# Optimization experiments

Measured on AMD Instinct MI355X. Metric: run time of the kernel, lower is better.

The kernel has to match this reference:

```python
import jax, jax.numpy as jnp
import numpy as np

B, N, D, D_MODEL = 4, 2048, 512, 512


def setup_inputs() -> dict:
    key = jax.random.key(0)
    kx, kq, kk, kv, ks = jax.random.split(key, 5)
    scale = 1.0 / np.sqrt(D)
    x = jax.random.normal(kx, (B, N, D), dtype=jnp.float32)
    Wq = (jax.random.normal(kq, (D, D_MODEL), dtype=jnp.float32) * scale)
    Wk = (jax.random.normal(kk, (D, D_MODEL), dtype=jnp.float32) * scale)
    Wv = (jax.random.normal(kv, (D, D_MODEL), dtype=jnp.float32) * scale)
    Ws = (jax.random.normal(ks, (D, 1), dtype=jnp.float32) * scale)
    return {"x": x, "Wq": Wq, "Wk": Wk, "Wv": Wv, "Ws": Ws}


def reference(x, Wq, Wk, Wv, Ws):
    # Projections (Linear, no bias)
    Q = x @ Wq                      # (B, N, d_model)
    K = x @ Wk                      # (B, N, d_model)
    V = x @ Wv                      # (B, N, d_model)
    sigma = x @ Ws                  # (B, N, 1)

    n = x.shape[1]
    dm = Wq.shape[1]

    # Prior association: Gaussian kernel over |i-j| distance, row-normalized
    idx = jnp.arange(n)
    dist = jnp.abs(idx[:, None] - idx[None, :]).astype(x.dtype)      # (N, N)
    inv_norm = 1.0 / (jnp.sqrt(2.0 * jnp.pi).astype(x.dtype) * jnp.abs(sigma))
    gaussian = inv_norm * jnp.exp(-0.5 * jnp.square(dist[None] / sigma))  # (B,N,N)
    P = gaussian / jnp.sum(gaussian, axis=-1, keepdims=True)

    # Series association: scaled dot-product softmax attention
    scores = jnp.einsum('bnd,bmd->bnm', Q, K) / jnp.sqrt(jnp.asarray(dm, x.dtype))
    S = jax.nn.softmax(scores, axis=-1)                               # (B,N,N)

    # Reconstruction
    Z = S @ V                                                          # (B,N,d_model)
    return (Z, P)
```

## Files before the change

kernel.cpp:

```cpp
#include <hip/hip_runtime.h>

typedef float f32x4 __attribute__((ext_vector_type(4)));
typedef short s16x8 __attribute__((ext_vector_type(8)));
typedef unsigned short us4 __attribute__((ext_vector_type(4)));

#define MFMA16(a, b, c) __builtin_amdgcn_mfma_f32_16x16x32_bf16(a, b, c, 0, 0, 0)

#define GLOAD_LDS16(gp, lp) __builtin_amdgcn_global_load_lds( \
    (__attribute__((address_space(1))) void*)(gp),            \
    (__attribute__((address_space(3))) void*)(lp), 16, 0, 0)

__device__ __forceinline__ unsigned short f2bf(float f) {
    union { float f; unsigned u; } v; v.f = f;
    unsigned r = v.u + 0x7fffu + ((v.u >> 16) & 1u);
    return (unsigned short)(r >> 16);
}

#define RP 136
#define SH128 (128 * RP)

__device__ __forceinline__ void gemm_core128_cnt(
    const unsigned short* __restrict__ Ab, size_t Astride,
    const unsigned short* __restrict__ Bb, size_t Bstride,
    int K, unsigned short* sh, int t, f32x4 acc[4][4])
{
    const int wave = t >> 6, lane = t & 63;
    const int c = lane & 15, quad = lane >> 4;
    const int wm = (wave >> 1) * 64, wn = (wave & 1) * 64;
    const int srow = t >> 2;
    const int scol = (t & 3) * 8;

    const unsigned short* ga = Ab + (size_t)srow * Astride + scol;
    const unsigned short* gb = Bb + (size_t)srow * Bstride + scol;

    GLOAD_LDS16(ga,                 sh + t * 8);
    GLOAD_LDS16(ga + 64 * Astride,  sh + 2048 + t * 8);
    GLOAD_LDS16(gb,                 sh + 4096 + t * 8);
    GLOAD_LDS16(gb + 64 * Bstride,  sh + 6144 + t * 8);
    if (32 < K) {
        GLOAD_LDS16(ga + 32,                 sh + 8192 + t * 8);
        GLOAD_LDS16(ga + 32 + 64 * Astride,  sh + 8192 + 2048 + t * 8);
        GLOAD_LDS16(gb + 32,                 sh + 8192 + 4096 + t * 8);
        GLOAD_LDS16(gb + 32 + 64 * Bstride,  sh + 8192 + 6144 + t * 8);
    }

    int cur = 0;
    for (int k0 = 0; k0 < K; k0 += 32) {
        if (k0 + 32 < K) asm volatile("s_waitcnt vmcnt(4)" ::: "memory");
        else             asm volatile("s_waitcnt vmcnt(0)" ::: "memory");
        __builtin_amdgcn_s_barrier();
        __builtin_amdgcn_sched_barrier(0);

        const unsigned short* buf = sh + cur * 8192;
        s16x8 af[4], bf[4];
        #pragma unroll
        for (int i = 0; i < 4; i++)
            af[i] = *(const s16x8*)(buf + (wm + i * 16 + c) * 32 + quad * 8);
        #pragma unroll
        for (int i = 0; i < 4; i++)
            bf[i] = *(const s16x8*)(buf + 4096 + (wn + i * 16 + c) * 32 + quad * 8);

        asm volatile("s_waitcnt lgkmcnt(0)" ::: "memory");
        __builtin_amdgcn_sched_barrier(0);

        #pragma unroll
        for (int mt = 0; mt < 4; mt++)
            #pragma unroll
            for (int nt = 0; nt < 4; nt++)
                acc[mt][nt] = MFMA16(af[mt], bf[nt], acc[mt][nt]);

        __builtin_amdgcn_s_barrier();
        __builtin_amdgcn_sched_barrier(0);

        if (k0 + 64 < K) {
            unsigned short* nb = sh + cur * 8192;
            GLOAD_LDS16(ga + k0 + 64,                 nb + t * 8);
            GLOAD_LDS16(ga + k0 + 64 + 64 * Astride,  nb + 2048 + t * 8);
            GLOAD_LDS16(gb + k0 + 64,                 nb + 4096 + t * 8);
            GLOAD_LDS16(gb + k0 + 64 + 64 * Bstride,  nb + 6144 + t * 8);
        }
        cur ^= 1;
    }
}

__global__ __launch_bounds__(256) void k_convert(
    const float* __restrict__ x, const float* __restrict__ wq,
    const float* __restrict__ wk, const float* __restrict__ wv,
    unsigned short* __restrict__ xbf, unsigned short* __restrict__ wt)
{
    __shared__ __align__(16) unsigned short lt[64][72];

    int bid = blockIdx.x, t = threadIdx.x;
    if (bid < 4096) {
        int gid = bid * 256 + t;
        float4 v = ((const float4*)x)[gid];
        us4 o = { f2bf(v.x), f2bf(v.y), f2bf(v.z), f2bf(v.w) };
        ((us4*)xbf)[gid] = o;
    } else {
        int idx = bid - 4096;
        int w = idx >> 6;
        int tile = idx & 63;
        int tk = tile >> 3, tn = tile & 7;
        const float* src = ((w == 0) ? wq : (w == 1) ? wk : wv)
                         + (size_t)(tk * 64) * 512 + tn * 64;

        int row = t >> 2;
        int c0 = (t & 3) * 16;
        const float4* s = (const float4*)(src + (size_t)row * 512 + c0);
        #pragma unroll
        for (int q = 0; q < 4; q++) {
            float4 v = s[q];
            lt[c0 + q * 4 + 0][row] = f2bf(v.x);
            lt[c0 + q * 4 + 1][row] = f2bf(v.y);
            lt[c0 + q * 4 + 2][row] = f2bf(v.z);
            lt[c0 + q * 4 + 3][row] = f2bf(v.w);
        }
        __syncthreads();

        int n = t >> 2;
        int k0 = (t & 3) * 16;
        s16x8 a = *(const s16x8*)&lt[n][k0];
        s16x8 b = *(const s16x8*)&lt[n][k0 + 8];
        unsigned short* dst = wt + (((size_t)(w * 512 + tn * 64 + n)) << 9)
                                 + tk * 64 + k0;
        *(s16x8*)dst = a;
        *(s16x8*)(dst + 8) = b;
    }
}

__global__ __launch_bounds__(256) void k_proj(
    const unsigned short* __restrict__ xbf, const unsigned short* __restrict__ wt,
    unsigned short* __restrict__ qbf, unsigned short* __restrict__ kbf,
    unsigned short* __restrict__ vtbf)
{
    __shared__ __align__(16) unsigned short sh[SH128];

    int t = threadIdx.x;
    int m0 = blockIdx.x * 128, n0 = blockIdx.y * 128;
    f32x4 acc[4][4] = {};

    gemm_core128_cnt(xbf + (size_t)m0 * 512, 512, wt + (size_t)n0 * 512, 512,
                     512, sh, t, acc);

    int wave = t >> 6, lane = t & 63, c = lane & 15, quad = lane >> 4;
    int wm = (wave >> 1) * 64, wn = (wave & 1) * 64;
    int sel = blockIdx.y >> 2;

    if (sel < 2) {
        unsigned short* dst = sel ? kbf : qbf;
        int ncol0 = n0 - sel * 512;
        #pragma unroll
        for (int mt = 0; mt < 4; mt++)
            #pragma unroll
            for (int nt = 0; nt < 4; nt++)
                #pragma unroll
                for (int r = 0; r < 4; r++)
                    sh[(wm + mt * 16 + quad * 4 + r) * RP + wn + nt * 16 + c]
                        = f2bf(acc[mt][nt][r]);
        __syncthreads();
        int rr = t >> 1, hh = (t & 1) * 64;
        const s16x8* sp = (const s16x8*)(sh + rr * RP + hh);
        s16x8* dp = (s16x8*)(dst + (size_t)(m0 + rr) * 512 + ncol0 + hh);
        s16x8 v[8];
        #pragma unroll
        for (int i = 0; i < 8; i++) v[i] = sp[i];
        #pragma unroll
        for (int i = 0; i < 8; i++) dp[i] = v[i];
    } else {
        #pragma unroll
        for (int mt = 0; mt < 4; mt++)
            #pragma unroll
            for (int nt = 0; nt < 4; nt++)
                #pragma unroll
                for (int r = 0; r < 4; r++)
                    sh[(wn + nt * 16 + c) * RP + wm + mt * 16 + quad * 4 + r]
                        = f2bf(acc[mt][nt][r]);
        __syncthreads();
        int bb = m0 >> 11, nn0 = m0 & 2047;
        int dbase = n0 - 1024;
        int dl = t >> 1, nh = (t & 1) * 64;
        const s16x8* sp = (const s16x8*)(sh + dl * RP + nh);
        s16x8* dp = (s16x8*)(vtbf + ((size_t)(bb * 512 + dbase + dl)) * 2048
                                  + nn0 + nh);
        s16x8 v[8];
        #pragma unroll
        for (int i = 0; i < 8; i++) v[i] = sp[i];
        #pragma unroll
        for (int i = 0; i < 8; i++) dp[i] = v[i];
    }
}

__device__ __forceinline__ void score_body(
    const unsigned short* __restrict__ qbf, const unsigned short* __restrict__ kbf,
    unsigned short* __restrict__ pbf,
    int b, int m0, int n0, int t, unsigned short* sh)
{
    f32x4 acc[4][4] = {};
    gemm_core128_cnt(qbf + (size_t)(b * 2048 + m0) * 512, 512,
                     kbf + (size_t)(b * 2048 + n0) * 512, 512,
                     512, sh, t, acc);

    int wave = t >> 6, lane = t & 63, c = lane & 15, quad = lane >> 4;
    int wm = (wave >> 1) * 64, wn = (wave & 1) * 64;
    const float scale = 0.044194173824159216f;

    #pragma unroll
    for (int mt = 0; mt < 4; mt++) {
        #pragma unroll
        for (int r = 0; r < 4; r++) {
            int row = wm + mt * 16 + quad * 4 + r;
            #pragma unroll
            for (int nt = 0; nt < 4; nt++) {
                float p = __expf(acc[mt][nt][r] * scale);
                sh[row * RP + wn + nt * 16 + c] = f2bf(p);
            }
        }
    }
    __syncthreads();
    int rr = t >> 1, hh = (t & 1) * 64;
    const s16x8* sp = (const s16x8*)(sh + rr * RP + hh);
    s16x8* dp = (s16x8*)(pbf + (size_t)(b * 2048 + m0 + rr) * 2048 + n0 + hh);
    s16x8 v[8];
    #pragma unroll
    for (int i = 0; i < 8; i++) v[i] = sp[i];
    #pragma unroll
    for (int i = 0; i < 8; i++) dp[i] = v[i];
}

__device__ __forceinline__ void prior_wave(
    const float* __restrict__ x, const float* __restrict__ wsv,
    float* __restrict__ pout, int row, int lane)
{
    const float4* xr = (const float4*)(x + (size_t)row * 512);
    const float4* wr = (const float4*)wsv;
    float4 a0 = xr[lane * 2],     b0 = wr[lane * 2];
    float4 a1 = xr[lane * 2 + 1], b1 = wr[lane * 2 + 1];
    float part = a0.x * b0.x + a0.y * b0.y + a0.z * b0.z + a0.w * b0.w
               + a1.x * b1.x + a1.y * b1.y + a1.z * b1.z + a1.w * b1.w;
    #pragma unroll
    for (int o = 32; o; o >>= 1) part += __shfl_xor(part, o, 64);
    float sigma = part;
    float inv2 = 0.5f / (sigma * sigma);

    int i = row & 2047;
    float g[32];
    float sum = 0.f;
    #pragma unroll
    for (int u = 0; u < 8; u++) {
        #pragma unroll
        for (int v = 0; v < 4; v++) {
            float d = (float)(u * 256 + lane * 4 + v - i);
            float e = __expf(-(d * d) * inv2);
            g[u * 4 + v] = e;
            sum += e;
        }
    }
    #pragma unroll
    for (int o = 32; o; o >>= 1) sum += __shfl_xor(sum, o, 64);
    float inv = 1.0f / sum;

    float4* pr = (float4*)(pout + (size_t)row * 2048);
    #pragma unroll
    for (int u = 0; u < 8; u++) {
        float4 o4 = { g[u * 4] * inv, g[u * 4 + 1] * inv,
                      g[u * 4 + 2] * inv, g[u * 4 + 3] * inv };
        pr[u * 64 + lane] = o4;
    }
}

__global__ __launch_bounds__(256) void k_score_prior(
    const unsigned short* __restrict__ qbf, const unsigned short* __restrict__ kbf,
    unsigned short* __restrict__ pbf,
    const float* __restrict__ x, const float* __restrict__ wsv,
    float* __restrict__ pout)
{
    __shared__ __align__(16) unsigned short sh[SH128];

    int bid = blockIdx.x, t = threadIdx.x;
    if (bid < 1024) {
        int b = bid >> 8, r = bid & 255;
        score_body(qbf, kbf, pbf, b, (r & 15) * 128, (r >> 4) * 128, t, sh);
    } else {
        int row = (bid - 1024) * 4 + (t >> 6);
        prior_wave(x, wsv, pout, row, t & 63);
    }
}

__global__ __launch_bounds__(256) void k_score(
    const unsigned short* __restrict__ qbf, const unsigned short* __restrict__ kbf,
    unsigned short* __restrict__ pbf)
{
    __shared__ __align__(16) unsigned short sh[SH128];
    score_body(qbf, kbf, pbf, blockIdx.z,
               blockIdx.x * 128, blockIdx.y * 128, threadIdx.x, sh);
}

__global__ __launch_bounds__(256) void k_out(
    const unsigned short* __restrict__ pbf, const unsigned short* __restrict__ vtbf,
    float* __restrict__ zout)
{
    __shared__ __align__(16) unsigned short sh[12288];

    int t = threadIdx.x;
    int b = blockIdx.z;
    int m0 = blockIdx.x * 128, n0 = blockIdx.y * 64;

    const int wave = t >> 6, lane = t & 63;
    const int c = lane & 15, quad = lane >> 4;
    const int wm = (wave >> 1) * 64, wn = (wave & 1) * 32;
    const int srow = t >> 2;
    const int scol = (t & 3) * 8;

    const unsigned short* ga = pbf + (size_t)(b * 2048 + m0 + srow) * 2048 + scol;
    const unsigned short* gb = vtbf + (size_t)(b * 512 + n0 + srow) * 2048 + scol;

    s16x8 ones;
    #pragma unroll
    for (int i = 0; i < 8; i++) ones[i] = (short)0x3F80;

    f32x4 acc[4][2] = {};
    f32x4 accl[4] = {};

    GLOAD_LDS16(ga,                  sh + t * 8);
    GLOAD_LDS16(ga + 64 * 2048,      sh + 2048 + t * 8);
    GLOAD_LDS16(gb,                  sh + 4096 + t * 8);
    GLOAD_LDS16(ga + 32,             sh + 6144 + t * 8);
    GLOAD_LDS16(ga + 32 + 64 * 2048, sh + 6144 + 2048 + t * 8);
    GLOAD_LDS16(gb + 32,             sh + 6144 + 4096 + t * 8);

    int cur = 0;
    for (int k0 = 0; k0 < 2048; k0 += 32) {
        if (k0 + 32 < 2048) asm volatile("s_waitcnt vmcnt(3)" ::: "memory");
        else                asm volatile("s_waitcnt vmcnt(0)" ::: "memory");
        __builtin_amdgcn_s_barrier();
        __builtin_amdgcn_sched_barrier(0);

        const unsigned short* buf = sh + cur * 6144;
        s16x8 af[4], bf[2];
        #pragma unroll
        for (int i = 0; i < 4; i++)
            af[i] = *(const s16x8*)(buf + (wm + i * 16 + c) * 32 + quad * 8);
        #pragma unroll
        for (int i = 0; i < 2; i++)
            bf[i] = *(const s16x8*)(buf + 4096 + (wn + i * 16 + c) * 32 + quad * 8);

        asm volatile("s_waitcnt lgkmcnt(0)" ::: "memory");
        __builtin_amdgcn_sched_barrier(0);

        #pragma unroll
        for (int mt = 0; mt < 4; mt++) {
            #pragma unroll
            for (int nt = 0; nt < 2; nt++)
                acc[mt][nt] = MFMA16(af[mt], bf[nt], acc[mt][nt]);
            accl[mt] = MFMA16(af[mt], ones, accl[mt]);
        }

        __builtin_amdgcn_s_barrier();
        __builtin_amdgcn_sched_barrier(0);

        if (k0 + 64 < 2048) {
            unsigned short* nb = sh + cur * 6144;
            GLOAD_LDS16(ga + k0 + 64,             nb + t * 8);
            GLOAD_LDS16(ga + k0 + 64 + 64 * 2048, nb + 2048 + t * 8);
            GLOAD_LDS16(gb + k0 + 64,             nb + 4096 + t * 8);
        }
        cur ^= 1;
    }

    #pragma unroll
    for (int mt = 0; mt < 4; mt++) {
        #pragma unroll
        for (int r = 0; r < 4; r++) {
            int row = wm + mt * 16 + quad * 4 + r;
            float inv = 1.0f / accl[mt][r];
            #pragma unroll
            for (int nt = 0; nt < 2; nt++) {
                zout[(size_t)(b * 2048 + m0 + row) * 512 + n0 + wn + nt * 16 + c]
                    = acc[mt][nt][r] * inv;
            }
        }
    }
}

__global__ __launch_bounds__(256) void k_prior(
    const float* __restrict__ x, const float* __restrict__ wsv,
    float* __restrict__ pout)
{
    int row = blockIdx.x * 4 + (threadIdx.x >> 6);
    prior_wave(x, wsv, pout, row, threadIdx.x & 63);
}

extern "C" void kernel_launch(void* const* d_in, const int* in_sizes, int n_in,
                              void* d_out, int out_size, void* d_ws, size_t ws_size,
                              hipStream_t stream)
{
    const float* x  = (const float*)d_in[0];
    const float* wq = (const float*)d_in[1];
    const float* wk = (const float*)d_in[2];
    const float* wv = (const float*)d_in[3];
    const float* ws = (const float*)d_in[4];

    float* zout = (float*)d_out;
    float* pout = zout + (size_t)4 * 2048 * 512;

    const size_t need = ((size_t)4194304 + 786432 + 3 * 4194304 + 16777216) * 2;

    if (ws_size >= need) {
        unsigned short* base = (unsigned short*)d_ws;
        unsigned short* xbf  = base;
        unsigned short* wt   = xbf  + (size_t)4194304;
        unsigned short* qbf  = wt   + (size_t)786432;
        unsigned short* kbf  = qbf  + (size_t)4194304;
        unsigned short* vtbf = kbf  + (size_t)4194304;
        unsigned short* pbf  = vtbf + (size_t)4194304;

        k_convert<<<dim3(4288), dim3(256), 0, stream>>>(x, wq, wk, wv, xbf, wt);
        k_proj       <<<dim3(64, 12),   dim3(256), 0, stream>>>(xbf, wt, qbf, kbf, vtbf);
        k_score_prior<<<dim3(3072),     dim3(256), 0, stream>>>(qbf, kbf, pbf, x, ws, pout);
        k_out        <<<dim3(16, 8, 4), dim3(256), 0, stream>>>(pbf, vtbf, zout);
    } else {
        unsigned short* base = (unsigned short*)pout;
        unsigned short* pbf  = base;
        unsigned short* qbf  = base + (size_t)16777216;
        unsigned short* kbf  = qbf  + (size_t)4194304;
        unsigned short* vtbf = kbf  + (size_t)4194304;
        unsigned short* xbf  = base;
        unsigned short* wt   = base + (size_t)4194304;

        k_convert<<<dim3(4288), dim3(256), 0, stream>>>(x, wq, wk, wv, xbf, wt);
        k_proj  <<<dim3(64, 12),    dim3(256), 0, stream>>>(xbf, wt, qbf, kbf, vtbf);
        k_score <<<dim3(16, 16, 4), dim3(256), 0, stream>>>(qbf, kbf, pbf);
        k_out   <<<dim3(16, 8, 4),  dim3(256), 0, stream>>>(pbf, vtbf, zout);
        k_prior <<<dim3(2048),      dim3(256), 0, stream>>>(x, ws, pout);
    }
}
```

Before: 198.2 us.

## Triple-buffer GEMM K-loops, swizzle block order, move prior into convert kernel

Every MFMA GEMM loop (projection, score, output) now keeps three LDS stages in flight instead of two, with vmcnt waits adjusted to match. This is meant to hide more global-load latency. Grids are flattened to 1D with an XCD-aware swizzle (blockIdx & 7) so that neighbouring tiles share L2 on the same die. The Gaussian prior computation moves out of the score kernel and into the convert kernel, so the score kernel runs GEMM only. The cost is more LDS per block (48 KB for the 128x128 GEMMs), which may reduce occupancy.

```diff
diff --git a/kernel.cpp b/kernel.cpp
--- a/kernel.cpp
+++ b/kernel.cpp
@@ -17,9 +17,9 @@
 }
 
 #define RP 136
-#define SH128 (128 * RP)
-
-__device__ __forceinline__ void gemm_core128_cnt(
+#define SH128 24576
+
+__device__ __forceinline__ void gemm_core128_p3(
     const unsigned short* __restrict__ Ab, size_t Astride,
     const unsigned short* __restrict__ Bb, size_t Bstride,
     int K, unsigned short* sh, int t, f32x4 acc[4][4])
@@ -32,33 +32,33 @@
 
     const unsigned short* ga = Ab + (size_t)srow * Astride + scol;
     const unsigned short* gb = Bb + (size_t)srow * Bstride + scol;
-
-    GLOAD_LDS16(ga,                 sh + t * 8);
-    GLOAD_LDS16(ga + 64 * Astride,  sh + 2048 + t * 8);
-    GLOAD_LDS16(gb,                 sh + 4096 + t * 8);
-    GLOAD_LDS16(gb + 64 * Bstride,  sh + 6144 + t * 8);
-    if (32 < K) {
-        GLOAD_LDS16(ga + 32,                 sh + 8192 + t * 8);
-        GLOAD_LDS16(ga + 32 + 64 * Astride,  sh + 8192 + 2048 + t * 8);
-        GLOAD_LDS16(gb + 32,                 sh + 8192 + 4096 + t * 8);
-        GLOAD_LDS16(gb + 32 + 64 * Bstride,  sh + 8192 + 6144 + t * 8);
+    const int nt = K >> 5;
+
+    for (int p = 0; p < 3 && p < nt; p++) {
+        unsigned short* nb = sh + p * 8192;
+        GLOAD_LDS16(ga + p * 32,                 nb + t * 8);
+        GLOAD_LDS16(ga + p * 32 + 64 * Astride,  nb + 2048 + t * 8);
+        GLOAD_LDS16(gb + p * 32,                 nb + 4096 + t * 8);
+        GLOAD_LDS16(gb + p * 32 + 64 * Bstride,  nb + 6144 + t * 8);
     }
 
     int cur = 0;
-    for (int k0 = 0; k0 < K; k0 += 32) {
-        if (k0 + 32 < K) asm volatile("s_waitcnt vmcnt(4)" ::: "memory");
-        else             asm volatile("s_waitcnt vmcnt(0)" ::: "memory");
+    for (int i = 0; i < nt; i++) {
+        int rem = nt - 1 - i;
+        if (rem >= 2)      asm volatile("s_waitcnt vmcnt(8)" ::: "memory");
+        else if (rem == 1) asm volatile("s_waitcnt vmcnt(4)" ::: "memory");
+        else               asm volatile("s_waitcnt vmcnt(0)" ::: "memory");
         __builtin_amdgcn_s_barrier();
         __builtin_amdgcn_sched_barrier(0);
 
         const unsigned short* buf = sh + cur * 8192;
         s16x8 af[4], bf[4];
         #pragma unroll
-        for (int i = 0; i < 4; i++)
-            af[i] = *(const s16x8*)(buf + (wm + i * 16 + c) * 32 + quad * 8);
-        #pragma unroll
-        for (int i = 0; i < 4; i++)
-            bf[i] = *(const s16x8*)(buf + 4096 + (wn + i * 16 + c) * 32 + quad * 8);
+        for (int q = 0; q < 4; q++)
+            af[q] = *(const s16x8*)(buf + (wm + q * 16 + c) * 32 + quad * 8);
+        #pragma unroll
+        for (int q = 0; q < 4; q++)
+            bf[q] = *(const s16x8*)(buf + 4096 + (wn + q * 16 + c) * 32 + quad * 8);
 
         asm volatile("s_waitcnt lgkmcnt(0)" ::: "memory");
         __builtin_amdgcn_sched_barrier(0);
@@ -66,31 +66,71 @@
         #pragma unroll
         for (int mt = 0; mt < 4; mt++)
             #pragma unroll
-            for (int nt = 0; nt < 4; nt++)
-                acc[mt][nt] = MFMA16(af[mt], bf[nt], acc[mt][nt]);
+            for (int ntl = 0; ntl < 4; ntl++)
+                acc[mt][ntl] = MFMA16(af[mt], bf[ntl], acc[mt][ntl]);
 
         __builtin_amdgcn_s_barrier();
         __builtin_amdgcn_sched_barrier(0);
 
-        if (k0 + 64 < K) {
+        if (i + 3 < nt) {
             unsigned short* nb = sh + cur * 8192;
-            GLOAD_LDS16(ga + k0 + 64,                 nb + t * 8);
-            GLOAD_LDS16(ga + k0 + 64 + 64 * Astride,  nb + 2048 + t * 8);
-            GLOAD_LDS16(gb + k0 + 64,                 nb + 4096 + t * 8);
-            GLOAD_LDS16(gb + k0 + 64 + 64 * Bstride,  nb + 6144 + t * 8);
-        }
-        cur ^= 1;
-    }
-}
-
-__global__ __launch_bounds__(256) void k_convert(
+            int kk = (i + 3) * 32;
+            GLOAD_LDS16(ga + kk,                 nb + t * 8);
+            GLOAD_LDS16(ga + kk + 64 * Astride,  nb + 2048 + t * 8);
+            GLOAD_LDS16(gb + kk,                 nb + 4096 + t * 8);
+            GLOAD_LDS16(gb + kk + 64 * Bstride,  nb + 6144 + t * 8);
+        }
+        cur = (cur == 2) ? 0 : cur + 1;
+    }
+}
+
+__device__ __forceinline__ void prior_wave(
+    const float* __restrict__ x, const float* __restrict__ wsv,
+    float* __restrict__ pout, int row, int lane)
+{
+    const float4* xr = (const float4*)(x + (size_t)row * 512);
+    const float4* wr = (const float4*)wsv;
+    float4 a0 = xr[lane * 2],     b0 = wr[lane * 2];
+    float4 a1 = xr[lane * 2 + 1], b1 = wr[lane * 2 + 1];
+    float part = a0.x * b0.x + a0.y * b0.y + a0.z * b0.z + a0.w * b0.w
+               + a1.x * b1.x + a1.y * b1.y + a1.z * b1.z + a1.w * b1.w;
+    #pragma unroll
+    for (int o = 32; o; o >>= 1) part += __shfl_xor(part, o, 64);
+    float sigma = part;
+    float inv2 = 0.5f / (sigma * sigma);
+
+    int i = row & 2047;
+    float g[32];
+    float sum = 0.f;
+    #pragma unroll
+    for (int u = 0; u < 8; u++) {
+        #pragma unroll
+        for (int v = 0; v < 4; v++) {
+            float d = (float)(u * 256 + lane * 4 + v - i);
+            float e = __expf(-(d * d) * inv2);
+            g[u * 4 + v] = e;
+            sum += e;
+        }
+    }
+    #pragma unroll
+    for (int o = 32; o; o >>= 1) sum += __shfl_xor(sum, o, 64);
+    float inv = 1.0f / sum;
+
+    float4* pr = (float4*)(pout + (size_t)row * 2048);
+    #pragma unroll
+    for (int u = 0; u < 8; u++) {
+        float4 o4 = { g[u * 4] * inv, g[u * 4 + 1] * inv,
+                      g[u * 4 + 2] * inv, g[u * 4 + 3] * inv };
+        pr[u * 64 + lane] = o4;
+    }
+}
+
+__device__ __forceinline__ void convert_body(
     const float* __restrict__ x, const float* __restrict__ wq,
     const float* __restrict__ wk, const float* __restrict__ wv,
-    unsigned short* __restrict__ xbf, unsigned short* __restrict__ wt)
-{
-    __shared__ __align__(16) unsigned short lt[64][72];
-
-    int bid = blockIdx.x, t = threadIdx.x;
+    unsigned short* __restrict__ xbf, unsigned short* __restrict__ wt,
+    int bid, int t, unsigned short (*lt)[72])
+{
     if (bid < 4096) {
         int gid = bid * 256 + t;
         float4 v = ((const float4*)x)[gid];
@@ -128,6 +168,31 @@
     }
 }
 
+__global__ __launch_bounds__(256) void k_convert_prior(
+    const float* __restrict__ x, const float* __restrict__ wq,
+    const float* __restrict__ wk, const float* __restrict__ wv,
+    unsigned short* __restrict__ xbf, unsigned short* __restrict__ wt,
+    const float* __restrict__ wsv, float* __restrict__ pout)
+{
+    __shared__ __align__(16) unsigned short lt[64][72];
+    int bid = blockIdx.x, t = threadIdx.x;
+    if (bid < 4288) {
+        convert_body(x, wq, wk, wv, xbf, wt, bid, t, lt);
+    } else {
+        int row = (bid - 4288) * 4 + (t >> 6);
+        prior_wave(x, wsv, pout, row, t & 63);
+    }
+}
+
+__global__ __launch_bounds__(256) void k_convert(
+    const float* __restrict__ x, const float* __restrict__ wq,
+    const float* __restrict__ wk, const float* __restrict__ wv,
+    unsigned short* __restrict__ xbf, unsigned short* __restrict__ wt)
+{
+    __shared__ __align__(16) unsigned short lt[64][72];
+    convert_body(x, wq, wk, wv, xbf, wt, blockIdx.x, threadIdx.x, lt);
+}
+
 __global__ __launch_bounds__(256) void k_proj(
     const unsigned short* __restrict__ xbf, const unsigned short* __restrict__ wt,
     unsigned short* __restrict__ qbf, unsigned short* __restrict__ kbf,
@@ -136,15 +201,18 @@
     __shared__ __align__(16) unsigned short sh[SH128];
 
     int t = threadIdx.x;
-    int m0 = blockIdx.x * 128, n0 = blockIdx.y * 128;
+    int lin = blockIdx.x;
+    int sw = (lin & 7) * 96 + (lin >> 3);
+    int mt_ = sw / 12, nt_ = sw % 12;
+    int m0 = mt_ * 128, n0 = nt_ * 128;
     f32x4 acc[4][4] = {};
 
-    gemm_core128_cnt(xbf + (size_t)m0 * 512, 512, wt + (size_t)n0 * 512, 512,
-                     512, sh, t, acc);
+    gemm_core128_p3(xbf + (size_t)m0 * 512, 512, wt + (size_t)n0 * 512, 512,
+                    512, sh, t, acc);
 
     int wave = t >> 6, lane = t & 63, c = lane & 15, quad = lane >> 4;
     int wm = (wave >> 1) * 64, wn = (wave & 1) * 64;
-    int sel = blockIdx.y >> 2;
+    int sel = nt_ >> 2;
 
     if (sel < 2) {
         unsigned short* dst = sel ? kbf : qbf;
@@ -190,15 +258,21 @@
     }
 }
 
-__device__ __forceinline__ void score_body(
+__global__ __launch_bounds__(256) void k_score(
     const unsigned short* __restrict__ qbf, const unsigned short* __restrict__ kbf,
-    unsigned short* __restrict__ pbf,
-    int b, int m0, int n0, int t, unsigned short* sh)
-{
+    unsigned short* __restrict__ pbf)
+{
+    __shared__ __align__(16) unsigned short sh[SH128];
+
+    int t = threadIdx.x;
+    int sw = (blockIdx.x & 7) * 128 + (blockIdx.x >> 3);
+    int b = sw >> 8, r = sw & 255;
+    int m0 = (r >> 4) * 128, n0 = (r & 15) * 128;
+
     f32x4 acc[4][4] = {};
-    gemm_core128_cnt(qbf + (size_t)(b * 2048 + m0) * 512, 512,
-                     kbf + (size_t)(b * 2048 + n0) * 512, 512,
-                     512, sh, t, acc);
+    gemm_core128_p3(qbf + (size_t)(b * 2048 + m0) * 512, 512,
+                    kbf + (size_t)(b * 2048 + n0) * 512, 512,
+                    512, sh, t, acc);
 
     int wave = t >> 6, lane = t & 63, c = lane & 15, quad = lane >> 4;
     int wm = (wave >> 1) * 64, wn = (wave & 1) * 64;
@@ -207,11 +281,11 @@
     #pragma unroll
     for (int mt = 0; mt < 4; mt++) {
         #pragma unroll
-        for (int r = 0; r < 4; r++) {
-            int row = wm + mt * 16 + quad * 4 + r;
+        for (int r2 = 0; r2 < 4; r2++) {
+            int row = wm + mt * 16 + quad * 4 + r2;
             #pragma unroll
             for (int nt = 0; nt < 4; nt++) {
-                float p = __expf(acc[mt][nt][r] * scale);
+                float p = __expf(acc[mt][nt][r2] * scale);
                 sh[row * RP + wn + nt * 16 + c] = f2bf(p);
             }
         }
@@ -227,83 +301,16 @@
     for (int i = 0; i < 8; i++) dp[i] = v[i];
 }
 
-__device__ __forceinline__ void prior_wave(
-    const float* __restrict__ x, const float* __restrict__ wsv,
-    float* __restrict__ pout, int row, int lane)
-{
-    const float4* xr = (const float4*)(x + (size_t)row * 512);
-    const float4* wr = (const float4*)wsv;
-    float4 a0 = xr[lane * 2],     b0 = wr[lane * 2];
-    float4 a1 = xr[lane * 2 + 1], b1 = wr[lane * 2 + 1];
-    float part = a0.x * b0.x + a0.y * b0.y + a0.z * b0.z + a0.w * b0.w
-               + a1.x * b1.x + a1.y * b1.y + a1.z * b1.z + a1.w * b1.w;
-    #pragma unroll
-    for (int o = 32; o; o >>= 1) part += __shfl_xor(part, o, 64);
-    float sigma = part;
-    float inv2 = 0.5f / (sigma * sigma);
-
-    int i = row & 2047;
-    float g[32];
-    float sum = 0.f;
-    #pragma unroll
-    for (int u = 0; u < 8; u++) {
-        #pragma unroll
-        for (int v = 0; v < 4; v++) {
-            float d = (float)(u * 256 + lane * 4 + v - i);
-            float e = __expf(-(d * d) * inv2);
-            g[u * 4 + v] = e;
-            sum += e;
-        }
-    }
-    #pragma unroll
-    for (int o = 32; o; o >>= 1) sum += __shfl_xor(sum, o, 64);
-    float inv = 1.0f / sum;
-
-    float4* pr = (float4*)(pout + (size_t)row * 2048);
-    #pragma unroll
-    for (int u = 0; u < 8; u++) {
-        float4 o4 = { g[u * 4] * inv, g[u * 4 + 1] * inv,
-                      g[u * 4 + 2] * inv, g[u * 4 + 3] * inv };
-        pr[u * 64 + lane] = o4;
-    }
-}
-
-__global__ __launch_bounds__(256) void k_score_prior(
-    const unsigned short* __restrict__ qbf, const unsigned short* __restrict__ kbf,
-    unsigned short* __restrict__ pbf,
-    const float* __restrict__ x, const float* __restrict__ wsv,
-    float* __restrict__ pout)
-{
-    __shared__ __align__(16) unsigned short sh[SH128];
-
-    int bid = blockIdx.x, t = threadIdx.x;
-    if (bid < 1024) {
-        int b = bid >> 8, r = bid & 255;
-        score_body(qbf, kbf, pbf, b, (r & 15) * 128, (r >> 4) * 128, t, sh);
-    } else {
-        int row = (bid - 1024) * 4 + (t >> 6);
-        prior_wave(x, wsv, pout, row, t & 63);
-    }
-}
-
-__global__ __launch_bounds__(256) void k_score(
-    const unsigned short* __restrict__ qbf, const unsigned short* __restrict__ kbf,
-    unsigned short* __restrict__ pbf)
-{
-    __shared__ __align__(16) unsigned short sh[SH128];
-    score_body(qbf, kbf, pbf, blockIdx.z,
-               blockIdx.x * 128, blockIdx.y * 128, threadIdx.x, sh);
-}
-
 __global__ __launch_bounds__(256) void k_out(
     const unsigned short* __restrict__ pbf, const unsigned short* __restrict__ vtbf,
     float* __restrict__ zout)
 {
-    __shared__ __align__(16) unsigned short sh[12288];
+    __shared__ __align__(16) unsigned short sh[18432];
 
     int t = threadIdx.x;
-    int b = blockIdx.z;
-    int m0 = blockIdx.x * 128, n0 = blockIdx.y * 64;
+    int sw = (blockIdx.x & 7) * 64 + (blockIdx.x >> 3);
+    int b = sw >> 7, r = sw & 127;
+    int m0 = (r >> 3) * 128, n0 = (r & 7) * 64;
 
     const int wave = t >> 6, lane = t & 63;
     const int c = lane & 15, quad = lane >> 4;
@@ -321,28 +328,31 @@
     f32x4 acc[4][2] = {};
     f32x4 accl[4] = {};
 
-    GLOAD_LDS16(ga,                  sh + t * 8);
-    GLOAD_LDS16(ga + 64 * 2048,      sh + 2048 + t * 8);
-    GLOAD_LDS16(gb,                  sh + 4096 + t * 8);
-    GLOAD_LDS16(ga + 32,             sh + 6144 + t * 8);
-    GLOAD_LDS16(ga + 32 + 64 * 2048, sh + 6144 + 2048 + t * 8);
-    GLOAD_LDS16(gb + 32,             sh + 6144 + 4096 + t * 8);
+    #pragma unroll
+    for (int p = 0; p < 3; p++) {
+        unsigned short* nb = sh + p * 6144;
+        GLOAD_LDS16(ga + p * 32,             nb + t * 8);
+        GLOAD_LDS16(ga + p * 32 + 64 * 2048, nb + 2048 + t * 8);
+        GLOAD_LDS16(gb + p * 32,             nb + 4096 + t * 8);
+    }
 
     int cur = 0;
-    for (int k0 = 0; k0 < 2048; k0 += 32) {
-        if (k0 + 32 < 2048) asm volatile("s_waitcnt vmcnt(3)" ::: "memory");
-        else                asm volatile("s_waitcnt vmcnt(0)" ::: "memory");
+    for (int i = 0; i < 64; i++) {
+        int rem = 63 - i;
+        if (rem >= 2)      asm volatile("s_waitcnt vmcnt(6)" ::: "memory");
+        else if (rem == 1) asm volatile("s_waitcnt vmcnt(3)" ::: "memory");
+        else               asm volatile("s_waitcnt vmcnt(0)" ::: "memory");
         __builtin_amdgcn_s_barrier();
         __builtin_amdgcn_sched_barrier(0);
 
         const unsigned short* buf = sh + cur * 6144;
         s16x8 af[4], bf[2];
         #pragma unroll
-        for (int i = 0; i < 4; i++)
-            af[i] = *(const s16x8*)(buf + (wm + i * 16 + c) * 32 + quad * 8);
-        #pragma unroll
-        for (int i = 0; i < 2; i++)
-            bf[i] = *(const s16x8*)(buf + 4096 + (wn + i * 16 + c) * 32 + quad * 8);
+        for (int q = 0; q < 4; q++)
+            af[q] = *(const s16x8*)(buf + (wm + q * 16 + c) * 32 + quad * 8);
+        #pragma unroll
+        for (int q = 0; q < 2; q++)
+            bf[q] = *(const s16x8*)(buf + 4096 + (wn + q * 16 + c) * 32 + quad * 8);
 
         asm volatile("s_waitcnt lgkmcnt(0)" ::: "memory");
         __builtin_amdgcn_sched_barrier(0);
@@ -358,25 +368,26 @@
         __builtin_amdgcn_s_barrier();
         __builtin_amdgcn_sched_barrier(0);
 
-        if (k0 + 64 < 2048) {
+        if (i + 3 < 64) {
             unsigned short* nb = sh + cur * 6144;
-            GLOAD_LDS16(ga + k0 + 64,             nb + t * 8);
-            GLOAD_LDS16(ga + k0 + 64 + 64 * 2048, nb + 2048 + t * 8);
-            GLOAD_LDS16(gb + k0 + 64,             nb + 4096 + t * 8);
-        }
-        cur ^= 1;
+            int kk = (i + 3) * 32;
+            GLOAD_LDS16(ga + kk,             nb + t * 8);
+            GLOAD_LDS16(ga + kk + 64 * 2048, nb + 2048 + t * 8);
+            GLOAD_LDS16(gb + kk,             nb + 4096 + t * 8);
+        }
+        cur = (cur == 2) ? 0 : cur + 1;
     }
 
     #pragma unroll
     for (int mt = 0; mt < 4; mt++) {
         #pragma unroll
-        for (int r = 0; r < 4; r++) {
-            int row = wm + mt * 16 + quad * 4 + r;
-            float inv = 1.0f / accl[mt][r];
+        for (int r2 = 0; r2 < 4; r2++) {
+            int row = wm + mt * 16 + quad * 4 + r2;
+            float inv = 1.0f / accl[mt][r2];
             #pragma unroll
             for (int nt = 0; nt < 2; nt++) {
                 zout[(size_t)(b * 2048 + m0 + row) * 512 + n0 + wn + nt * 16 + c]
-                    = acc[mt][nt][r] * inv;
+                    = acc[mt][nt][r2] * inv;
             }
         }
     }
@@ -414,10 +425,11 @@
         unsigned short* vtbf = kbf  + (size_t)4194304;
         unsigned short* pbf  = vtbf + (size_t)4194304;
 
-        k_convert<<<dim3(4288), dim3(256), 0, stream>>>(x, wq, wk, wv, xbf, wt);
-        k_proj       <<<dim3(64, 12),   dim3(256), 0, stream>>>(xbf, wt, qbf, kbf, vtbf);
-        k_score_prior<<<dim3(3072),     dim3(256), 0, stream>>>(qbf, kbf, pbf, x, ws, pout);
-        k_out        <<<dim3(16, 8, 4), dim3(256), 0, stream>>>(pbf, vtbf, zout);
+        k_convert_prior<<<dim3(6336), dim3(256), 0, stream>>>(
+            x, wq, wk, wv, xbf, wt, ws, pout);
+        k_proj <<<dim3(768),  dim3(256), 0, stream>>>(xbf, wt, qbf, kbf, vtbf);
+        k_score<<<dim3(1024), dim3(256), 0, stream>>>(qbf, kbf, pbf);
+        k_out  <<<dim3(512),  dim3(256), 0, stream>>>(pbf, vtbf, zout);
     } else {
         unsigned short* base = (unsigned short*)pout;
         unsigned short* pbf  = base;
@@ -428,9 +440,9 @@
         unsigned short* wt   = base + (size_t)4194304;
 
         k_convert<<<dim3(4288), dim3(256), 0, stream>>>(x, wq, wk, wv, xbf, wt);
-        k_proj  <<<dim3(64, 12),    dim3(256), 0, stream>>>(xbf, wt, qbf, kbf, vtbf);
-        k_score <<<dim3(16, 16, 4), dim3(256), 0, stream>>>(qbf, kbf, pbf);
-        k_out   <<<dim3(16, 8, 4),  dim3(256), 0, stream>>>(pbf, vtbf, zout);
-        k_prior <<<dim3(2048),      dim3(256), 0, stream>>>(x, ws, pout);
-    }
-}
+        k_proj <<<dim3(768),  dim3(256), 0, stream>>>(xbf, wt, qbf, kbf, vtbf);
+        k_score<<<dim3(1024), dim3(256), 0, stream>>>(qbf, kbf, pbf);
+        k_out  <<<dim3(512),  dim3(256), 0, stream>>>(pbf, vtbf, zout);
+        k_prior<<<dim3(2048), dim3(256), 0, stream>>>(x, ws, pout);
+    }
+}
```

Result: slower. 203.1 us (+2.5%).

## Enlarge projection and score GEMM tiles to 256x256 with 512-thread blocks

Applied to the files above, without the earlier changes.

Replaces the 128x128 GEMM core with a 256x256 tile computed by 8 waves, each holding 128x64 of accumulators. This raises arithmetic intensity and cuts global/LDS traffic per FLOP for the projection and score kernels. It also drops the LDS-staged epilogue in favour of direct scalar bf16 stores to global memory. The prior rows are re-batched to 8 per block. The larger tile means more accumulator registers, fewer blocks (256 score blocks on a 256-CU part), and uncoalesced 2-byte epilogue stores, so occupancy and store efficiency may suffer.

```diff
diff --git a/kernel.cpp b/kernel.cpp
--- a/kernel.cpp
+++ b/kernel.cpp
@@ -16,55 +16,55 @@
     return (unsigned short)(r >> 16);
 }
 
-#define RP 136
-#define SH128 (128 * RP)
-
-__device__ __forceinline__ void gemm_core128_cnt(
+__device__ __forceinline__ void gemm_core256(
     const unsigned short* __restrict__ Ab, size_t Astride,
     const unsigned short* __restrict__ Bb, size_t Bstride,
-    int K, unsigned short* sh, int t, f32x4 acc[4][4])
-{
-    const int wave = t >> 6, lane = t & 63;
+    int K, unsigned short* sh, int t, f32x4 acc[8][4])
+{
+    const int w = t >> 6, lane = t & 63;
     const int c = lane & 15, quad = lane >> 4;
-    const int wm = (wave >> 1) * 64, wn = (wave & 1) * 64;
+    const int arow = (w >> 2) * 128;
+    const int brow = (w & 3) * 64;
     const int srow = t >> 2;
     const int scol = (t & 3) * 8;
 
     const unsigned short* ga = Ab + (size_t)srow * Astride + scol;
     const unsigned short* gb = Bb + (size_t)srow * Bstride + scol;
-
-    GLOAD_LDS16(ga,                 sh + t * 8);
-    GLOAD_LDS16(ga + 64 * Astride,  sh + 2048 + t * 8);
-    GLOAD_LDS16(gb,                 sh + 4096 + t * 8);
-    GLOAD_LDS16(gb + 64 * Bstride,  sh + 6144 + t * 8);
-    if (32 < K) {
-        GLOAD_LDS16(ga + 32,                 sh + 8192 + t * 8);
-        GLOAD_LDS16(ga + 32 + 64 * Astride,  sh + 8192 + 2048 + t * 8);
-        GLOAD_LDS16(gb + 32,                 sh + 8192 + 4096 + t * 8);
-        GLOAD_LDS16(gb + 32 + 64 * Bstride,  sh + 8192 + 6144 + t * 8);
-    }
+    const int ntil = K >> 5;
+
+#define STAGE256(p, bbuf) do {                                      \
+        unsigned short* nb = sh + (bbuf) * 16384;                   \
+        int kk = (p) * 32;                                          \
+        GLOAD_LDS16(ga + kk,                 nb + t * 8);           \
+        GLOAD_LDS16(ga + kk + 128 * Astride, nb + 4096 + t * 8);    \
+        GLOAD_LDS16(gb + kk,                 nb + 8192 + t * 8);    \
+        GLOAD_LDS16(gb + kk + 128 * Bstride, nb + 12288 + t * 8);   \
+    } while (0)
+
+    STAGE256(0, 0);
+    STAGE256(1, 1);
 
     int cur = 0;
-    for (int k0 = 0; k0 < K; k0 += 32) {
-        if (k0 + 32 < K) asm volatile("s_waitcnt vmcnt(4)" ::: "memory");
-        else             asm volatile("s_waitcnt vmcnt(0)" ::: "memory");
+    for (int i = 0; i < ntil; i++) {
+        if (i + 1 < ntil) asm volatile("s_waitcnt vmcnt(4)" ::: "memory");
+        else              asm volatile("s_waitcnt vmcnt(0)" ::: "memory");
         __builtin_amdgcn_s_barrier();
         __builtin_amdgcn_sched_barrier(0);
 
-        const unsigned short* buf = sh + cur * 8192;
-        s16x8 af[4], bf[4];
-        #pragma unroll
-        for (int i = 0; i < 4; i++)
-            af[i] = *(const s16x8*)(buf + (wm + i * 16 + c) * 32 + quad * 8);
-        #pragma unroll
-        for (int i = 0; i < 4; i++)
-            bf[i] = *(const s16x8*)(buf + 4096 + (wn + i * 16 + c) * 32 + quad * 8);
+        const unsigned short* buf = sh + cur * 16384;
+        s16x8 af[8], bf[4];
+        #pragma unroll
+        for (int q = 0; q < 8; q++)
+            af[q] = *(const s16x8*)(buf + (arow + q * 16 + c) * 32 + quad * 8);
+        #pragma unroll
+        for (int q = 0; q < 4; q++)
+            bf[q] = *(const s16x8*)(buf + 8192 + (brow + q * 16 + c) * 32 + quad * 8);
 
         asm volatile("s_waitcnt lgkmcnt(0)" ::: "memory");
         __builtin_amdgcn_sched_barrier(0);
 
         #pragma unroll
-        for (int mt = 0; mt < 4; mt++)
+        for (int mt = 0; mt < 8; mt++)
             #pragma unroll
             for (int nt = 0; nt < 4; nt++)
                 acc[mt][nt] = MFMA16(af[mt], bf[nt], acc[mt][nt]);
@@ -72,14 +72,50 @@
         __builtin_amdgcn_s_barrier();
         __builtin_amdgcn_sched_barrier(0);
 
-        if (k0 + 64 < K) {
-            unsigned short* nb = sh + cur * 8192;
-            GLOAD_LDS16(ga + k0 + 64,                 nb + t * 8);
-            GLOAD_LDS16(ga + k0 + 64 + 64 * Astride,  nb + 2048 + t * 8);
-            GLOAD_LDS16(gb + k0 + 64,                 nb + 4096 + t * 8);
-            GLOAD_LDS16(gb + k0 + 64 + 64 * Bstride,  nb + 6144 + t * 8);
-        }
+        if (i + 2 < ntil) STAGE256(i + 2, cur);
         cur ^= 1;
+    }
+#undef STAGE256
+}
+
+__device__ __forceinline__ void prior_wave(
+    const float* __restrict__ x, const float* __restrict__ wsv,
+    float* __restrict__ pout, int row, int lane)
+{
+    const float4* xr = (const float4*)(x + (size_t)row * 512);
+    const float4* wr = (const float4*)wsv;
+    float4 a0 = xr[lane * 2],     b0 = wr[lane * 2];
+    float4 a1 = xr[lane * 2 + 1], b1 = wr[lane * 2 + 1];
+    float part = a0.x * b0.x + a0.y * b0.y + a0.z * b0.z + a0.w * b0.w
+               + a1.x * b1.x + a1.y * b1.y + a1.z * b1.z + a1.w * b1.w;
+    #pragma unroll
+    for (int o = 32; o; o >>= 1) part += __shfl_xor(part, o, 64);
+    float sigma = part;
+    float inv2 = 0.5f / (sigma * sigma);
+
+    int i = row & 2047;
+    float g[32];
+    float sum = 0.f;
+    #pragma unroll
+    for (int u = 0; u < 8; u++) {
+        #pragma unroll
+        for (int v = 0; v < 4; v++) {
+            float d = (float)(u * 256 + lane * 4 + v - i);
+            float e = __expf(-(d * d) * inv2);
+            g[u * 4 + v] = e;
+            sum += e;
+        }
+    }
+    #pragma unroll
+    for (int o = 32; o; o >>= 1) sum += __shfl_xor(sum, o, 64);
+    float inv = 1.0f / sum;
+
+    float4* pr = (float4*)(pout + (size_t)row * 2048);
+    #pragma unroll
+    for (int u = 0; u < 8; u++) {
+        float4 o4 = { g[u * 4] * inv, g[u * 4 + 1] * inv,
+                      g[u * 4 + 2] * inv, g[u * 4 + 3] * inv };
+        pr[u * 64 + lane] = o4;
     }
 }
 
@@ -128,65 +164,53 @@
     }
 }
 
-__global__ __launch_bounds__(256) void k_proj(
+__global__ __launch_bounds__(512, 2) void k_proj(
     const unsigned short* __restrict__ xbf, const unsigned short* __restrict__ wt,
     unsigned short* __restrict__ qbf, unsigned short* __restrict__ kbf,
     unsigned short* __restrict__ vtbf)
 {
-    __shared__ __align__(16) unsigned short sh[SH128];
+    __shared__ __align__(16) unsigned short sh[32768];
 
     int t = threadIdx.x;
-    int m0 = blockIdx.x * 128, n0 = blockIdx.y * 128;
-    f32x4 acc[4][4] = {};
-
-    gemm_core128_cnt(xbf + (size_t)m0 * 512, 512, wt + (size_t)n0 * 512, 512,
-                     512, sh, t, acc);
-
-    int wave = t >> 6, lane = t & 63, c = lane & 15, quad = lane >> 4;
-    int wm = (wave >> 1) * 64, wn = (wave & 1) * 64;
-    int sel = blockIdx.y >> 2;
+    int mt_ = blockIdx.x / 6, nt_ = blockIdx.x % 6;
+    int m0 = mt_ * 256, n0 = nt_ * 256;
+
+    f32x4 acc[8][4] = {};
+    gemm_core256(xbf + (size_t)m0 * 512, 512, wt + (size_t)n0 * 512, 512,
+                 512, sh, t, acc);
+
+    int w = t >> 6, lane = t & 63, c = lane & 15, quad = lane >> 4;
+    int wr = w >> 2, wc = w & 3;
+    int sel = nt_ >> 1;
 
     if (sel < 2) {
         unsigned short* dst = sel ? kbf : qbf;
         int ncol0 = n0 - sel * 512;
         #pragma unroll
-        for (int mt = 0; mt < 4; mt++)
-            #pragma unroll
-            for (int nt = 0; nt < 4; nt++)
+        for (int mt = 0; mt < 8; mt++) {
+            #pragma unroll
+            for (int nt = 0; nt < 4; nt++) {
+                int col = ncol0 + wc * 64 + nt * 16 + c;
                 #pragma unroll
-                for (int r = 0; r < 4; r++)
-                    sh[(wm + mt * 16 + quad * 4 + r) * RP + wn + nt * 16 + c]
-                        = f2bf(acc[mt][nt][r]);
-        __syncthreads();
-        int rr = t >> 1, hh = (t & 1) * 64;
-        const s16x8* sp = (const s16x8*)(sh + rr * RP + hh);
-        s16x8* dp = (s16x8*)(dst + (size_t)(m0 + rr) * 512 + ncol0 + hh);
-        s16x8 v[8];
-        #pragma unroll
-        for (int i = 0; i < 8; i++) v[i] = sp[i];
-        #pragma unroll
-        for (int i = 0; i < 8; i++) dp[i] = v[i];
+                for (int r = 0; r < 4; r++) {
+                    int rw = m0 + wr * 128 + mt * 16 + quad * 4 + r;
+                    dst[(size_t)rw * 512 + col] = f2bf(acc[mt][nt][r]);
+                }
+            }
+        }
     } else {
         #pragma unroll
-        for (int mt = 0; mt < 4; mt++)
-            #pragma unroll
-            for (int nt = 0; nt < 4; nt++)
-                #pragma unroll
-                for (int r = 0; r < 4; r++)
-                    sh[(wn + nt * 16 + c) * RP + wm + mt * 16 + quad * 4 + r]
-                        = f2bf(acc[mt][nt][r]);
-        __syncthreads();
-        int bb = m0 >> 11, nn0 = m0 & 2047;
-        int dbase = n0 - 1024;
-        int dl = t >> 1, nh = (t & 1) * 64;
-        const s16x8* sp = (const s16x8*)(sh + dl * RP + nh);
-        s16x8* dp = (s16x8*)(vtbf + ((size_t)(bb * 512 + dbase + dl)) * 2048
-                                  + nn0 + nh);
-        s16x8 v[8];
-        #pragma unroll
-        for (int i = 0; i < 8; i++) v[i] = sp[i];
-        #pragma unroll
-        for (int i = 0; i < 8; i++) dp[i] = v[i];
+        for (int mt = 0; mt < 8; mt++) {
+            int rw0 = m0 + wr * 128 + mt * 16 + quad * 4;
+            int bb = rw0 >> 11, nn = rw0 & 2047;
+            #pragma unroll
+            for (int nt = 0; nt < 4; nt++) {
+                int d = (n0 - 1024) + wc * 64 + nt * 16 + c;
+                us4 pk = { f2bf(acc[mt][nt][0]), f2bf(acc[mt][nt][1]),
+                           f2bf(acc[mt][nt][2]), f2bf(acc[mt][nt][3]) };
+                *(us4*)(vtbf + ((size_t)(bb * 512 + d)) * 2048 + nn) = pk;
+            }
+        }
     }
 }
 
@@ -195,104 +219,57 @@
     unsigned short* __restrict__ pbf,
     int b, int m0, int n0, int t, unsigned short* sh)
 {
-    f32x4 acc[4][4] = {};
-    gemm_core128_cnt(qbf + (size_t)(b * 2048 + m0) * 512, 512,
-                     kbf + (size_t)(b * 2048 + n0) * 512, 512,
-                     512, sh, t, acc);
-
-    int wave = t >> 6, lane = t & 63, c = lane & 15, quad = lane >> 4;
-    int wm = (wave >> 1) * 64, wn = (wave & 1) * 64;
+    f32x4 acc[8][4] = {};
+    gemm_core256(qbf + (size_t)(b * 2048 + m0) * 512, 512,
+                 kbf + (size_t)(b * 2048 + n0) * 512, 512,
+                 512, sh, t, acc);
+
+    int w = t >> 6, lane = t & 63, c = lane & 15, quad = lane >> 4;
+    int wr = w >> 2, wc = w & 3;
     const float scale = 0.044194173824159216f;
 
     #pragma unroll
-    for (int mt = 0; mt < 4; mt++) {
-        #pragma unroll
-        for (int r = 0; r < 4; r++) {
-            int row = wm + mt * 16 + quad * 4 + r;
-            #pragma unroll
-            for (int nt = 0; nt < 4; nt++) {
-                float p = __expf(acc[mt][nt][r] * scale);
-                sh[row * RP + wn + nt * 16 + c] = f2bf(p);
+    for (int mt = 0; mt < 8; mt++) {
+        #pragma unroll
+        for (int nt = 0; nt < 4; nt++) {
+            int col = n0 + wc * 64 + nt * 16 + c;
+            #pragma unroll
+            for (int r = 0; r < 4; r++) {
+                int row = m0 + wr * 128 + mt * 16 + quad * 4 + r;
+                pbf[(size_t)(b * 2048 + row) * 2048 + col]
+                    = f2bf(__expf(acc[mt][nt][r] * scale));
             }
         }
     }
-    __syncthreads();
-    int rr = t >> 1, hh = (t & 1) * 64;
-    const s16x8* sp = (const s16x8*)(sh + rr * RP + hh);
-    s16x8* dp = (s16x8*)(pbf + (size_t)(b * 2048 + m0 + rr) * 2048 + n0 + hh);
-    s16x8 v[8];
-    #pragma unroll
-    for (int i = 0; i < 8; i++) v[i] = sp[i];
-    #pragma unroll
-    for (int i = 0; i < 8; i++) dp[i] = v[i];
-}
-
-__device__ __forceinline__ void prior_wave(
-    const float* __restrict__ x, const float* __restrict__ wsv,
-    float* __restrict__ pout, int row, int lane)
-{
-    const float4* xr = (const float4*)(x + (size_t)row * 512);
-    const float4* wr = (const float4*)wsv;
-    float4 a0 = xr[lane * 2],     b0 = wr[lane * 2];
-    float4 a1 = xr[lane * 2 + 1], b1 = wr[lane * 2 + 1];
-    float part = a0.x * b0.x + a0.y * b0.y + a0.z * b0.z + a0.w * b0.w
-               + a1.x * b1.x + a1.y * b1.y + a1.z * b1.z + a1.w * b1.w;
-    #pragma unroll
-    for (int o = 32; o; o >>= 1) part += __shfl_xor(part, o, 64);
-    float sigma = part;
-    float inv2 = 0.5f / (sigma * sigma);
-
-    int i = row & 2047;
-    float g[32];
-    float sum = 0.f;
-    #pragma unroll
-    for (int u = 0; u < 8; u++) {
-        #pragma unroll
-        for (int v = 0; v < 4; v++) {
-            float d = (float)(u * 256 + lane * 4 + v - i);
-            float e = __expf(-(d * d) * inv2);
-            g[u * 4 + v] = e;
-            sum += e;
-        }
-    }
-    #pragma unroll
-    for (int o = 32; o; o >>= 1) sum += __shfl_xor(sum, o, 64);
-    float inv = 1.0f / sum;
-
-    float4* pr = (float4*)(pout + (size_t)row * 2048);
-    #pragma unroll
-    for (int u = 0; u < 8; u++) {
-        float4 o4 = { g[u * 4] * inv, g[u * 4 + 1] * inv,
-                      g[u * 4 + 2] * inv, g[u * 4 + 3] * inv };
-        pr[u * 64 + lane] = o4;
-    }
-}
-
-__global__ __launch_bounds__(256) void k_score_prior(
+}
+
+__global__ __launch_bounds__(512, 2) void k_score_prior(
     const unsigned short* __restrict__ qbf, const unsigned short* __restrict__ kbf,
     unsigned short* __restrict__ pbf,
     const float* __restrict__ x, const float* __restrict__ wsv,
     float* __restrict__ pout)
 {
-    __shared__ __align__(16) unsigned short sh[SH128];
+    __shared__ __align__(16) unsigned short sh[32768];
 
     int bid = blockIdx.x, t = threadIdx.x;
-    if (bid < 1024) {
-        int b = bid >> 8, r = bid & 255;
-        score_body(qbf, kbf, pbf, b, (r & 15) * 128, (r >> 4) * 128, t, sh);
+    if (bid < 256) {
+        int b = bid >> 6, r = bid & 63;
+        score_body(qbf, kbf, pbf, b, ((r >> 3) & 7) * 256, (r & 7) * 256, t, sh);
     } else {
-        int row = (bid - 1024) * 4 + (t >> 6);
+        int row = (bid - 256) * 8 + (t >> 6);
         prior_wave(x, wsv, pout, row, t & 63);
     }
 }
 
-__global__ __launch_bounds__(256) void k_score(
+__global__ __launch_bounds__(512, 2) void k_score(
     const unsigned short* __restrict__ qbf, const unsigned short* __restrict__ kbf,
     unsigned short* __restrict__ pbf)
 {
-    __shared__ __align__(16) unsigned short sh[SH128];
-    score_body(qbf, kbf, pbf, blockIdx.z,
-               blockIdx.x * 128, blockIdx.y * 128, threadIdx.x, sh);
+    __shared__ __align__(16) unsigned short sh[32768];
+    int bid = blockIdx.x;
+    int b = bid >> 6, r = bid & 63;
+    score_body(qbf, kbf, pbf, b, ((r >> 3) & 7) * 256, (r & 7) * 256,
+               threadIdx.x, sh);
 }
 
 __global__ __launch_bounds__(256) void k_out(
@@ -382,11 +359,11 @@
     }
 }
 
-__global__ __launch_bounds__(256) void k_prior(
+__global__ __launch_bounds__(512) void k_prior(
     const float* __restrict__ x, const float* __restrict__ wsv,
     float* __restrict__ pout)
 {
-    int row = blockIdx.x * 4 + (threadIdx.x >> 6);
+    int row = blockIdx.x * 8 + (threadIdx.x >> 6);
     prior_wave(x, wsv, pout, row, threadIdx.x & 63);
 }
 
@@ -415,8 +392,8 @@
         unsigned short* pbf  = vtbf + (size_t)4194304;
 
         k_convert<<<dim3(4288), dim3(256), 0, stream>>>(x, wq, wk, wv, xbf, wt);
-        k_proj       <<<dim3(64, 12),   dim3(256), 0, stream>>>(xbf, wt, qbf, kbf, vtbf);
-        k_score_prior<<<dim3(3072),     dim3(256), 0, stream>>>(qbf, kbf, pbf, x, ws, pout);
+        k_proj       <<<dim3(192),      dim3(512), 0, stream>>>(xbf, wt, qbf, kbf, vtbf);
+        k_score_prior<<<dim3(1280),     dim3(512), 0, stream>>>(qbf, kbf, pbf, x, ws, pout);
         k_out        <<<dim3(16, 8, 4), dim3(256), 0, stream>>>(pbf, vtbf, zout);
     } else {
         unsigned short* base = (unsigned short*)pout;
@@ -428,9 +405,9 @@
         unsigned short* wt   = base + (size_t)4194304;
 
         k_convert<<<dim3(4288), dim3(256), 0, stream>>>(x, wq, wk, wv, xbf, wt);
-        k_proj  <<<dim3(64, 12),    dim3(256), 0, stream>>>(xbf, wt, qbf, kbf, vtbf);
-        k_score <<<dim3(16, 16, 4), dim3(256), 0, stream>>>(qbf, kbf, pbf);
-        k_out   <<<dim3(16, 8, 4),  dim3(256), 0, stream>>>(pbf, vtbf, zout);
-        k_prior <<<dim3(2048),      dim3(256), 0, stream>>>(x, ws, pout);
-    }
-}
+        k_proj <<<dim3(192),      dim3(512), 0, stream>>>(xbf, wt, qbf, kbf, vtbf);
+        k_score<<<dim3(256),      dim3(512), 0, stream>>>(qbf, kbf, pbf);
+        k_out  <<<dim3(16, 8, 4), dim3(256), 0, stream>>>(pbf, vtbf, zout);
+        k_prior<<<dim3(1024),     dim3(512), 0, stream>>>(x, ws, pout);
+    }
+}
```

Measured after the change: 191.4 us. 1.04x faster.
